# Kernel tuning notes

Hardware: AMD Instinct MI355X
Metric: run time of the kernel (lower is better)

Reference implementation:

```python
import jax, jax.numpy as jnp
import numpy as np

N_NODES = 100000
N_EDGES = 3200000
NUM_GRAPHS = 2048
IN_CH = 35
HID = 128
EPS = 1e-5


def setup_inputs() -> dict:
    key = jax.random.key(0)
    ks = jax.random.split(key, 16)
    x = jax.random.normal(ks[0], (N_NODES, IN_CH), dtype=jnp.float32)
    edge_index = jax.random.randint(ks[1], (2, N_EDGES), 0, N_NODES, dtype=jnp.int64)
    batch = jnp.sort(jax.random.randint(ks[2], (N_NODES,), 0, NUM_GRAPHS, dtype=jnp.int64))
    def lin(k, fan_in, fan_out):
        b = 1.0 / np.sqrt(fan_in)
        kw, kb = jax.random.split(k)
        W = jax.random.uniform(kw, (fan_in, fan_out), minval=-b, maxval=b, dtype=jnp.float32)
        bias = jax.random.uniform(kb, (fan_out,), minval=-b, maxval=b, dtype=jnp.float32)
        return W, bias
    W1, b1 = lin(ks[3], IN_CH, HID)
    W2, b2 = lin(ks[4], HID, HID)
    W3, b3 = lin(ks[5], HID, HID)
    Wl1, bl1 = lin(ks[6], HID, HID // 2)
    Wl2, bl2 = lin(ks[7], HID // 2, 1)
    ones = jnp.ones((HID,), jnp.float32)
    zeros = jnp.zeros((HID,), jnp.float32)
    return {
        'x': x, 'edge_index': edge_index, 'batch': batch,
        'W1': W1, 'b1': b1, 'g1': ones, 'be1': zeros,
        'W2': W2, 'b2': b2, 'g2': ones, 'be2': zeros,
        'W3': W3, 'b3': b3, 'g3': ones, 'be3': zeros,
        'Wl1': Wl1, 'bl1': bl1, 'Wl2': Wl2, 'bl2': bl2,
    }


def _gcn_norm(edge_index, n):
    # add self-loops, compute symmetric normalization D^-1/2 (A+I) D^-1/2
    loop = jnp.arange(n, dtype=edge_index.dtype)
    src = jnp.concatenate([edge_index[0], loop])
    dst = jnp.concatenate([edge_index[1], loop])
    deg = jax.ops.segment_sum(jnp.ones_like(dst, jnp.float32), dst, num_segments=n)
    dinv = jnp.where(deg > 0, jax.lax.rsqrt(deg), 0.0)
    norm = dinv[src] * dinv[dst]
    return src, dst, norm


def _gcn_conv(x, src, dst, norm, W, b):
    h = x @ W                      # [N, out]
    msg = h[src] * norm[:, None]   # gather + scale (irregular)
    out = jax.ops.segment_sum(msg, dst, num_segments=x.shape[0])
    return out + b


def _bn(x, g, be):
    mu = jnp.mean(x, axis=0)
    var = jnp.mean(jnp.square(x - mu), axis=0)  # biased var (torch BN training)
    return (x - mu) * jax.lax.rsqrt(var + EPS) * g + be


def reference(x, edge_index, batch, W1, b1, g1, be1, W2, b2, g2, be2,
              W3, b3, g3, be3, Wl1, bl1, Wl2, bl2):
    n = x.shape[0]
    src, dst, norm = _gcn_norm(edge_index, n)
    h = jax.nn.gelu(_bn(_gcn_conv(x, src, dst, norm, W1, b1), g1, be1), approximate=False)
    h = jax.nn.gelu(_bn(_gcn_conv(h, src, dst, norm, W2, b2), g2, be2), approximate=False)
    h = jax.nn.gelu(_bn(_gcn_conv(h, src, dst, norm, W3, b3), g3, be3), approximate=False)
    # global mean pool by graph id
    s = jax.ops.segment_sum(h, batch, num_segments=NUM_GRAPHS)
    cnt = jax.ops.segment_sum(jnp.ones((n,), jnp.float32), batch, num_segments=NUM_GRAPHS)
    pooled = s / jnp.maximum(cnt, 1.0)[:, None]
    out = jax.nn.elu(pooled @ Wl1 + bl1)
    out = out @ Wl2 + bl2
    return out  # [NUM_GRAPHS, 1]
```

## Files before the change

### kernel.cpp

```cpp
#include <hip/hip_runtime.h>
#include <hip/hip_bf16.h>
#include <math.h>

#define N_NODES 100000
#define N_EDGES 3200000
#define NUM_GRAPHS 2048
#define IN_CH 35
#define HID 128
#define BN_EPS 1e-5f

#define BUCK_SHIFT 9
#define BUCK_SIZE 512
#define NB_BUCK 196
#define BIN_GRID 1024
#define BIN_CHUNK 3125

__device__ __forceinline__ float gelu_f(float x) {
    return 0.5f * x * (1.0f + erff(x * 0.70710678118654752440f));
}

__device__ __forceinline__ float bflo(unsigned v) { return __uint_as_float(v << 16); }
__device__ __forceinline__ float bfhi(unsigned v) { return __uint_as_float(v & 0xffff0000u); }
__device__ __forceinline__ unsigned f2bf(float f) {
    unsigned x = __float_as_uint(f);
    return (x + 0x7fffu + ((x >> 16) & 1u)) >> 16;
}
__device__ __forceinline__ unsigned packbf2(float lo, float hi) {
    return f2bf(lo) | (f2bf(hi) << 16);
}


__global__ void k_zero2(int* __restrict__ bcnt, float* __restrict__ stats,
                        unsigned* __restrict__ xzero, unsigned* __restrict__ hzero) {
    int i = threadIdx.x;
    if (i < NB_BUCK) bcnt[i] = 0;
    if (i < 3 * 256) stats[i] = 0.0f;
    if (i < 32) xzero[i] = 0u;
    if (i < 64) hzero[i] = 0u;
}


__global__ void k_bhist(const int* __restrict__ ei, int* __restrict__ bcnt) {
    __shared__ int hist[NB_BUCK];
    int tid = threadIdx.x;
    if (tid < NB_BUCK) hist[tid] = 0;
    __syncthreads();
    int e0 = blockIdx.x * BIN_CHUNK;
    int e1 = min(e0 + BIN_CHUNK, N_EDGES);
    for (int e = e0 + tid; e < e1; e += 256) {
        int d = ei[N_EDGES + e];
        atomicAdd(&hist[d >> BUCK_SHIFT], 1);
    }
    __syncthreads();
    if (tid < NB_BUCK && hist[tid] > 0) atomicAdd(&bcnt[tid], hist[tid]);
}


__global__ void k_bscan(const int* __restrict__ bcnt, int* __restrict__ bbase,
                        int* __restrict__ bcursor, int* __restrict__ rowp) {
    __shared__ int sa[256];
    __shared__ int sb[256];
    int tid = threadIdx.x;
    sa[tid] = (tid < NB_BUCK) ? bcnt[tid] : 0;
    __syncthreads();
    int* src = sa; int* dst = sb;
    for (int st = 1; st < 256; st <<= 1) {
        int v = src[tid];
        if (tid >= st) v += src[tid - st];
        dst[tid] = v;
        __syncthreads();
        int* t = src; src = dst; dst = t;
    }
    if (tid < NB_BUCK) {
        int ex = (tid == 0) ? 0 : src[tid - 1];
        bbase[tid] = ex;
        bcursor[tid] = ex;
    }
    if (tid == 0) {
        bbase[NB_BUCK] = N_EDGES;
        rowp[N_NODES] = N_EDGES;
    }
}


__global__ void k_bin(const int* __restrict__ ei, int* __restrict__ bcursor,
                      int2* __restrict__ edges) {
    __shared__ int lsrc[BIN_CHUNK];
    __shared__ int ldst[BIN_CHUNK];
    __shared__ int hist[NB_BUCK];
    __shared__ int hbase[NB_BUCK];
    __shared__ int lcur[NB_BUCK];
    int tid = threadIdx.x;
    if (tid < NB_BUCK) { hist[tid] = 0; lcur[tid] = 0; }
    __syncthreads();
    int e0 = blockIdx.x * BIN_CHUNK;
    int nE = min(e0 + BIN_CHUNK, N_EDGES) - e0;
    for (int i = tid; i < nE; i += 256) {
        int s = ei[e0 + i];
        int d = ei[N_EDGES + e0 + i];
        lsrc[i] = s;
        ldst[i] = d;
        atomicAdd(&hist[d >> BUCK_SHIFT], 1);
    }
    __syncthreads();
    if (tid < NB_BUCK) {
        int h = hist[tid];
        hbase[tid] = (h > 0) ? atomicAdd(&bcursor[tid], h) : 0;
    }
    __syncthreads();
    for (int i = tid; i < nE; i += 256) {
        int d = ldst[i];
        int b = d >> BUCK_SHIFT;
        int off = atomicAdd(&lcur[b], 1);
        edges[hbase[b] + off] = make_int2(lsrc[i], d);
    }
}


__global__ void k_fill(const int* __restrict__ bbase, const int2* __restrict__ edges,
                       int* __restrict__ rowp, float* __restrict__ dinv,
                       int* __restrict__ col) {
    __shared__ int ldeg[BUCK_SIZE];
    __shared__ int sa[BUCK_SIZE];
    __shared__ int sb[BUCK_SIZE];
    __shared__ int lcur[BUCK_SIZE];
    int b = blockIdx.x;
    int tid = threadIdx.x;
    int base_node = b << BUCK_SHIFT;
    int nn = min(BUCK_SIZE, N_NODES - base_node);
    int seg0 = bbase[b];
    int seg1 = bbase[b + 1];
    ldeg[tid] = 0;
    __syncthreads();
    for (int e = seg0 + tid; e < seg1; e += BUCK_SIZE) {
        atomicAdd(&ldeg[edges[e].y - base_node], 1);
    }
    __syncthreads();
    sa[tid] = ldeg[tid];
    __syncthreads();
    int* src = sa; int* dst = sb;
    for (int st = 1; st < BUCK_SIZE; st <<= 1) {
        int v = src[tid];
        if (tid >= st) v += src[tid - st];
        dst[tid] = v;
        __syncthreads();
        int* t = src; src = dst; dst = t;
    }
    int ex = (tid == 0) ? 0 : src[tid - 1];
    int rp = seg0 + ex;
    lcur[tid] = rp;
    if (tid < nn) {
        rowp[base_node + tid] = rp;
        dinv[base_node + tid] = rsqrtf((float)(ldeg[tid] + 1));
    }
    __syncthreads();
    for (int e = seg0 + tid; e < seg1; e += BUCK_SIZE) {
        int2 sd = edges[e];
        int p = atomicAdd(&lcur[sd.y - base_node], 1);
        col[p] = sd.x;
    }
}


__global__ void k_castx(const float* __restrict__ X, const float* __restrict__ dinv,
                        unsigned* __restrict__ Xb) {
    int i = blockIdx.x * blockDim.x + threadIdx.x;
    if (i >= N_NODES * 32) return;
    int n = i >> 5, j = i & 31;
    float dv = dinv[n];
    float lo = 0.0f, hi = 0.0f;
    if (j < 17) {
        lo = X[(size_t)n * IN_CH + 2 * j];
        hi = X[(size_t)n * IN_CH + 2 * j + 1];
    } else if (j == 17) {
        lo = X[(size_t)n * IN_CH + 34];
    }
    Xb[i] = packbf2(dv * lo, dv * hi);
}

#define ACC8(v) { a0 += bflo(v.x); a1 += bfhi(v.x); a2 += bflo(v.y); a3 += bfhi(v.y); \
                  a4 += bflo(v.z); a5 += bfhi(v.z); a6 += bflo(v.w); a7 += bfhi(v.w); }
#define ACC4(v) { a0 += bflo(v.x); a1 += bfhi(v.x); a2 += bflo(v.y); a3 += bfhi(v.y); }


#define C1_NODES 8

__global__ __launch_bounds__(512) void k_conv1(
        const unsigned* __restrict__ Xb, const int* __restrict__ rowp,
        const int* __restrict__ col, const float* __restrict__ dinv,
        const float* __restrict__ W1, const float* __restrict__ b1,
        unsigned* __restrict__ Yb) {
    __shared__ float w_s[IN_CH * HID];
    __shared__ float b_s[HID];
    __shared__ float xa_s[C1_NODES][36];
    int tid = threadIdx.x;
    for (int u = tid; u < IN_CH * HID; u += 512) w_s[u] = W1[u];
    if (tid < HID) b_s[tid] = b1[tid];

    int wid = tid >> 6;
    int lane = tid & 63;
    int g = lane >> 4;
    int j = lane & 15;
    int node = blockIdx.x * C1_NODES + wid;
    bool valid = node < N_NODES;

    float a0 = 0.0f, a1 = 0.0f, a2 = 0.0f, a3 = 0.0f;
    float di = 0.0f;
    if (valid) {
        int rp0 = rowp[node], rp1 = rowp[node + 1];
        di = dinv[node];
        uint2 sv = *(const uint2*)(Xb + (size_t)node * 32 + j * 2);
        float w0 = (g == 0) ? 1.0f : 0.0f;
        a0 = w0 * bflo(sv.x); a1 = w0 * bfhi(sv.x);
        a2 = w0 * bflo(sv.y); a3 = w0 * bfhi(sv.y);
        unsigned deg = (unsigned)(rp1 - rp0);
        for (int e0 = (rp0 & ~3); e0 < rp1; e0 += 16) {
            int eb = e0 + 4 * g;
            int4 cs = *(const int4*)(col + eb);
            int s0 = ((unsigned)(eb + 0 - rp0) < deg) ? cs.x : N_NODES;
            int s1 = ((unsigned)(eb + 1 - rp0) < deg) ? cs.y : N_NODES;
            int s2 = ((unsigned)(eb + 2 - rp0) < deg) ? cs.z : N_NODES;
            int s3 = ((unsigned)(eb + 3 - rp0) < deg) ? cs.w : N_NODES;
            uint2 v0 = *(const uint2*)(Xb + (size_t)s0 * 32 + j * 2);
            uint2 v1 = *(const uint2*)(Xb + (size_t)s1 * 32 + j * 2);
            uint2 v2 = *(const uint2*)(Xb + (size_t)s2 * 32 + j * 2);
            uint2 v3 = *(const uint2*)(Xb + (size_t)s3 * 32 + j * 2);
            ACC4(v0); ACC4(v1); ACC4(v2); ACC4(v3);
        }
    }
    a0 += __shfl(a0, (lane + 32) & 63, 64);
    a1 += __shfl(a1, (lane + 32) & 63, 64);
    a2 += __shfl(a2, (lane + 32) & 63, 64);
    a3 += __shfl(a3, (lane + 32) & 63, 64);
    a0 += __shfl(a0, (lane + 16) & 63, 64);
    a1 += __shfl(a1, (lane + 16) & 63, 64);
    a2 += __shfl(a2, (lane + 16) & 63, 64);
    a3 += __shfl(a3, (lane + 16) & 63, 64);
    if (valid && g == 0 && j < 9) {
        xa_s[wid][4 * j + 0] = di * a0;
        xa_s[wid][4 * j + 1] = di * a1;
        xa_s[wid][4 * j + 2] = di * a2;
        xa_s[wid][4 * j + 3] = di * a3;
    }
    __syncthreads();
    float acc0 = b_s[2 * lane];
    float acc1 = b_s[2 * lane + 1];
    #pragma unroll 7
    for (int k = 0; k < IN_CH; ++k) {
        float xv = xa_s[wid][k];
        acc0 = fmaf(xv, w_s[k * HID + 2 * lane], acc0);
        acc1 = fmaf(xv, w_s[k * HID + 2 * lane + 1], acc1);
    }
    if (valid) Yb[(size_t)node * 64 + lane] = packbf2(acc0, acc1);
}


__global__ void k_gemm128(const unsigned* __restrict__ Yb, const float* __restrict__ stats,
                          const float* __restrict__ g, const float* __restrict__ be,
                          const float* __restrict__ W, const float* __restrict__ dinv,
                          unsigned* __restrict__ Hb) {
    __shared__ float xs[32 * HID];
    __shared__ float sc_s[HID];
    __shared__ float sh_s[HID];
    int tid = threadIdx.x;
    if (tid < HID) {
        const float inv_n = 1.0f / (float)N_NODES;
        float mean = stats[tid] * inv_n;
        float var = stats[HID + tid] * inv_n - mean * mean;
        float s = g[tid] * rsqrtf(var + BN_EPS);
        sc_s[tid] = s;
        sh_s[tid] = be[tid] - mean * s;
    }
    __syncthreads();
    int row0 = blockIdx.x * 32;
    for (int u = tid; u < 32 * 64; u += 256) {
        int r = u >> 6, p = u & 63;
        int gr = row0 + r;
        float lo = 0.0f, hi = 0.0f;
        if (gr < N_NODES) {
            unsigned v = Yb[(size_t)gr * 64 + p];
            lo = gelu_f(fmaf(bflo(v), sc_s[2 * p], sh_s[2 * p]));
            hi = gelu_f(fmaf(bfhi(v), sc_s[2 * p + 1], sh_s[2 * p + 1]));
        }
        xs[r * HID + 2 * p]     = lo;
        xs[r * HID + 2 * p + 1] = hi;
    }
    __syncthreads();
    int tx = tid & 31, ty = tid >> 5;
    float acc[4][4] = {};
    for (int k = 0; k < HID; ++k) {
        float4 w = *(const float4*)&W[k * HID + tx * 4];
        #pragma unroll
        for (int rr = 0; rr < 4; ++rr) {
            float x = xs[(ty * 4 + rr) * HID + k];
            acc[rr][0] = fmaf(x, w.x, acc[rr][0]);
            acc[rr][1] = fmaf(x, w.y, acc[rr][1]);
            acc[rr][2] = fmaf(x, w.z, acc[rr][2]);
            acc[rr][3] = fmaf(x, w.w, acc[rr][3]);
        }
    }
    #pragma unroll
    for (int rr = 0; rr < 4; ++rr) {
        int gr = row0 + ty * 4 + rr;
        if (gr < N_NODES) {
            float dv = dinv[gr];
            unsigned lo = packbf2(dv * acc[rr][0], dv * acc[rr][1]);
            unsigned hi = packbf2(dv * acc[rr][2], dv * acc[rr][3]);
            *(uint2*)&Hb[(size_t)gr * 64 + tx * 2] = make_uint2(lo, hi);
        }
    }
}


__global__ void k_convb(const unsigned* __restrict__ Hb, const int* __restrict__ rowp,
                        const int* __restrict__ col, const float* __restrict__ dinv,
                        const float* __restrict__ bias, unsigned* __restrict__ Yb) {
    int tid = threadIdx.x;
    int wid = tid >> 6;
    int lane = tid & 63;
    int g = lane >> 4;
    int j = lane & 15;
    int node = blockIdx.x * 4 + wid;
    if (node >= N_NODES) return;
    int rp0 = rowp[node], rp1 = rowp[node + 1];
    float di = dinv[node];
    uint4 sv = *(const uint4*)(Hb + (size_t)node * 64 + j * 4);
    float w0 = (g == 0) ? 1.0f : 0.0f;
    float a0 = w0 * bflo(sv.x), a1 = w0 * bfhi(sv.x);
    float a2 = w0 * bflo(sv.y), a3 = w0 * bfhi(sv.y);
    float a4 = w0 * bflo(sv.z), a5 = w0 * bfhi(sv.z);
    float a6 = w0 * bflo(sv.w), a7 = w0 * bfhi(sv.w);
    unsigned deg = (unsigned)(rp1 - rp0);
    for (int e0 = (rp0 & ~3); e0 < rp1; e0 += 16) {
        int eb = e0 + 4 * g;
        int4 cs = *(const int4*)(col + eb);
        int s0 = ((unsigned)(eb + 0 - rp0) < deg) ? cs.x : N_NODES;
        int s1 = ((unsigned)(eb + 1 - rp0) < deg) ? cs.y : N_NODES;
        int s2 = ((unsigned)(eb + 2 - rp0) < deg) ? cs.z : N_NODES;
        int s3 = ((unsigned)(eb + 3 - rp0) < deg) ? cs.w : N_NODES;
        uint4 v0 = *(const uint4*)(Hb + (size_t)s0 * 64 + j * 4);
        uint4 v1 = *(const uint4*)(Hb + (size_t)s1 * 64 + j * 4);
        uint4 v2 = *(const uint4*)(Hb + (size_t)s2 * 64 + j * 4);
        uint4 v3 = *(const uint4*)(Hb + (size_t)s3 * 64 + j * 4);
        ACC8(v0); ACC8(v1); ACC8(v2); ACC8(v3);
    }
    a0 += __shfl(a0, (lane + 32) & 63, 64);
    a1 += __shfl(a1, (lane + 32) & 63, 64);
    a2 += __shfl(a2, (lane + 32) & 63, 64);
    a3 += __shfl(a3, (lane + 32) & 63, 64);
    a4 += __shfl(a4, (lane + 32) & 63, 64);
    a5 += __shfl(a5, (lane + 32) & 63, 64);
    a6 += __shfl(a6, (lane + 32) & 63, 64);
    a7 += __shfl(a7, (lane + 32) & 63, 64);
    a0 += __shfl(a0, (lane + 16) & 63, 64);
    a1 += __shfl(a1, (lane + 16) & 63, 64);
    a2 += __shfl(a2, (lane + 16) & 63, 64);
    a3 += __shfl(a3, (lane + 16) & 63, 64);
    a4 += __shfl(a4, (lane + 16) & 63, 64);
    a5 += __shfl(a5, (lane + 16) & 63, 64);
    a6 += __shfl(a6, (lane + 16) & 63, 64);
    a7 += __shfl(a7, (lane + 16) & 63, 64);
    if (g == 0) {
        const float4* bp = (const float4*)(bias + 8 * j);
        float4 bA = bp[0], bB = bp[1];
        uint4 o;
        o.x = packbf2(fmaf(di, a0, bA.x), fmaf(di, a1, bA.y));
        o.y = packbf2(fmaf(di, a2, bA.z), fmaf(di, a3, bA.w));
        o.z = packbf2(fmaf(di, a4, bB.x), fmaf(di, a5, bB.y));
        o.w = packbf2(fmaf(di, a6, bB.z), fmaf(di, a7, bB.w));
        *(uint4*)(Yb + (size_t)node * 64 + j * 4) = o;
    }
}


__global__ void k_statsb(const unsigned* __restrict__ Yb, float* __restrict__ stats) {
    __shared__ float ls[128];
    __shared__ float lss[128];
    int tid = threadIdx.x;
    int lane = tid & 63, grp = tid >> 6;
    if (tid < 128) { ls[tid] = 0.0f; lss[tid] = 0.0f; }
    __syncthreads();
    float s0 = 0, s1 = 0, q0 = 0, q1 = 0;
    for (int r = blockIdx.x * 4 + grp; r < N_NODES; r += gridDim.x * 4) {
        unsigned v = Yb[(size_t)r * 64 + lane];
        float lo = bflo(v), hi = bfhi(v);
        s0 += lo; q0 = fmaf(lo, lo, q0);
        s1 += hi; q1 = fmaf(hi, hi, q1);
    }
    atomicAdd(&ls[2 * lane], s0);
    atomicAdd(&ls[2 * lane + 1], s1);
    atomicAdd(&lss[2 * lane], q0);
    atomicAdd(&lss[2 * lane + 1], q1);
    __syncthreads();
    if (tid < 128) {
        atomicAdd(&stats[tid], ls[tid]);
        atomicAdd(&stats[128 + tid], lss[tid]);
    }
}


__device__ __forceinline__ int lowerb(const int* __restrict__ arr, int n, int key) {
    int lo = 0, hi = n;
    while (lo < hi) {
        int mid = (lo + hi) >> 1;
        if (arr[mid] < key) lo = mid + 1; else hi = mid;
    }
    return lo;
}

__global__ void k_pool_mlp(const unsigned* __restrict__ Yb, const float* __restrict__ stats,
                           const float* __restrict__ g, const float* __restrict__ be,
                           const int* __restrict__ batch,
                           const float* __restrict__ Wl1, const float* __restrict__ bl1,
                           const float* __restrict__ Wl2, const float* __restrict__ bl2,
                           float* __restrict__ out) {
    __shared__ float pooled[128];
    __shared__ float sc_s[128];
    __shared__ float sh_s[128];
    __shared__ int bounds[2];
    int gidx = blockIdx.x;
    int tid = threadIdx.x;
    if (tid < 128) {
        const float inv_n = 1.0f / (float)N_NODES;
        float mean = stats[tid] * inv_n;
        float var = stats[128 + tid] * inv_n - mean * mean;
        float s = g[tid] * rsqrtf(var + BN_EPS);
        sc_s[tid] = s;
        sh_s[tid] = be[tid] - mean * s;
    }
    if (tid == 0) {
        bounds[0] = lowerb(batch, N_NODES, gidx);
        bounds[1] = lowerb(batch, N_NODES, gidx + 1);
    }
    __syncthreads();
    int lo = bounds[0], hi = bounds[1];
    float s = sc_s[tid], h = sh_s[tid];
    int half = tid & 1;
    int word = tid >> 1;
    float acc = 0.0f;
    for (int r = lo; r < hi; ++r) {
        unsigned v = Yb[(size_t)r * 64 + word];
        float x = half ? bfhi(v) : bflo(v);
        acc += gelu_f(fmaf(x, s, h));
    }
    pooled[tid] = (hi > lo) ? acc / (float)(hi - lo) : 0.0f;
    __syncthreads();
    if (tid < 64) {
        float hs = bl1[tid];
        #pragma unroll 4
        for (int k = 0; k < 128; ++k)
            hs = fmaf(pooled[k], Wl1[k * 64 + tid], hs);
        float e = (hs > 0.0f) ? hs : expm1f(hs);
        float part = e * Wl2[tid];
        #pragma unroll
        for (int o = 32; o > 0; o >>= 1)
            part += __shfl_down(part, o);
        if (tid == 0) out[gidx] = part + bl2[0];
    }
}


extern "C" void kernel_launch(void* const* d_in, const int* in_sizes, int n_in,
                              void* d_out, int out_size, void* d_ws, size_t ws_size,
                              hipStream_t stream) {
    const float* x   = (const float*)d_in[0];
    const int*   ei  = (const int*)d_in[1];
    const int*   bat = (const int*)d_in[2];
    const float* W1  = (const float*)d_in[3];
    const float* b1  = (const float*)d_in[4];
    const float* g1  = (const float*)d_in[5];
    const float* be1 = (const float*)d_in[6];
    const float* W2  = (const float*)d_in[7];
    const float* b2  = (const float*)d_in[8];
    const float* g2  = (const float*)d_in[9];
    const float* be2 = (const float*)d_in[10];
    const float* W3  = (const float*)d_in[11];
    const float* b3  = (const float*)d_in[12];
    const float* g3  = (const float*)d_in[13];
    const float* be3 = (const float*)d_in[14];
    const float* Wl1 = (const float*)d_in[15];
    const float* bl1 = (const float*)d_in[16];
    const float* Wl2 = (const float*)d_in[17];
    const float* bl2 = (const float*)d_in[18];
    float* out = (float*)d_out;

    char* ws = (char*)d_ws;
    size_t off = 0;
    auto alloc = [&](size_t bytes) -> char* {
        char* p = ws + off;
        off += (bytes + 255) & ~(size_t)255;
        return p;
    };
    int*      bcnt    = (int*)alloc(NB_BUCK * sizeof(int));
    int*      bbase   = (int*)alloc((NB_BUCK + 1) * sizeof(int));
    int*      bcursor = (int*)alloc(NB_BUCK * sizeof(int));
    int2*     edges   = (int2*)alloc((size_t)N_EDGES * sizeof(int2));
    int*      rowp    = (int*)alloc((N_NODES + 1) * sizeof(int));
    float*    dinv    = (float*)alloc(N_NODES * sizeof(float));
    int*      col     = (int*)alloc((size_t)N_EDGES * sizeof(int));
    unsigned* Xb      = (unsigned*)alloc((size_t)(N_NODES + 1) * 32 * sizeof(unsigned));
    unsigned* Ybuf    = (unsigned*)alloc((size_t)N_NODES * 64 * sizeof(unsigned));
    unsigned* Hbuf    = (unsigned*)alloc((size_t)(N_NODES + 1) * 64 * sizeof(unsigned));
    float*    stats   = (float*)alloc(3 * 256 * sizeof(float));

    k_zero2<<<1, 1024, 0, stream>>>(bcnt, stats, Xb + (size_t)N_NODES * 32,
                                    Hbuf + (size_t)N_NODES * 64);
    k_bhist<<<BIN_GRID, 256, 0, stream>>>(ei, bcnt);
    k_bscan<<<1, 256, 0, stream>>>(bcnt, bbase, bcursor, rowp);
    k_bin<<<BIN_GRID, 256, 0, stream>>>(ei, bcursor, edges);
    k_fill<<<NB_BUCK, BUCK_SIZE, 0, stream>>>(bbase, edges, rowp, dinv, col);
    k_castx<<<(N_NODES * 32 + 255) / 256, 256, 0, stream>>>(x, dinv, Xb);

    const int gemm_blocks = (N_NODES + 31) / 32;
    const int conv_blocks = (N_NODES + 3) / 4;

    k_conv1<<<(N_NODES + C1_NODES - 1) / C1_NODES, 512, 0, stream>>>(
        Xb, rowp, col, dinv, W1, b1, Ybuf);
    k_statsb<<<1024, 256, 0, stream>>>(Ybuf, stats + 0 * 256);

    k_gemm128<<<gemm_blocks, 256, 0, stream>>>(Ybuf, stats + 0 * 256, g1, be1, W2, dinv, Hbuf);
    k_convb<<<conv_blocks, 256, 0, stream>>>(Hbuf, rowp, col, dinv, b2, Ybuf);
    k_statsb<<<1024, 256, 0, stream>>>(Ybuf, stats + 1 * 256);

    k_gemm128<<<gemm_blocks, 256, 0, stream>>>(Ybuf, stats + 1 * 256, g2, be2, W3, dinv, Hbuf);
    k_convb<<<conv_blocks, 256, 0, stream>>>(Hbuf, rowp, col, dinv, b3, Ybuf);
    k_statsb<<<1024, 256, 0, stream>>>(Ybuf, stats + 2 * 256);

    k_pool_mlp<<<NUM_GRAPHS, 128, 0, stream>>>(Ybuf, stats + 2 * 256, g3, be3, bat,
                                               Wl1, bl1, Wl2, bl2, out);
}
```

Measured before the change: 792.9 us.

## Use bf16 MFMA for hidden-layer GEMMs with pre-transposed bf16 weights

Replaces the scalar fp32 FMA 128x128 GEMM with a 64-row tile using the mfma_f32_16x16x32_bf16 instruction. BN+GELU activations are packed to bf16 into swizzled shared memory. Weights are cast and transposed once into bf16 by a new small kernel. This cuts the compute cost of the two GEMM stages. In exchange the weights lose precision to bf16 and the output stores are 16-bit scattered writes.

```diff
diff --git a/kernel.cpp b/kernel.cpp
--- a/kernel.cpp
+++ b/kernel.cpp
@@ -14,6 +14,9 @@
 #define NB_BUCK 196
 #define BIN_GRID 1024
 #define BIN_CHUNK 3125
+
+typedef short bf16x8 __attribute__((ext_vector_type(8)));
+typedef float f32x4 __attribute__((ext_vector_type(4)));
 
 __device__ __forceinline__ float gelu_f(float x) {
     return 0.5f * x * (1.0f + erff(x * 0.70710678118654752440f));
@@ -37,6 +40,18 @@
     if (i < 3 * 256) stats[i] = 0.0f;
     if (i < 32) xzero[i] = 0u;
     if (i < 64) hzero[i] = 0u;
+}
+
+
+__global__ void k_wcast(const float* __restrict__ W2, const float* __restrict__ W3,
+                        unsigned* __restrict__ Wt2, unsigned* __restrict__ Wt3) {
+    int t = blockIdx.x * 256 + threadIdx.x;
+    if (t >= 2 * 8192) return;
+    const float* W = (t < 8192) ? W2 : W3;
+    unsigned* Wt = (t < 8192) ? Wt2 : Wt3;
+    int i = t & 8191;
+    int n = i >> 6, j = i & 63;
+    Wt[n * 64 + j] = packbf2(W[(2 * j) * HID + n], W[(2 * j + 1) * HID + n]);
 }
 
 
@@ -255,11 +270,12 @@
 }
 
 
-__global__ void k_gemm128(const unsigned* __restrict__ Yb, const float* __restrict__ stats,
-                          const float* __restrict__ g, const float* __restrict__ be,
-                          const float* __restrict__ W, const float* __restrict__ dinv,
-                          unsigned* __restrict__ Hb) {
-    __shared__ float xs[32 * HID];
+__global__ __launch_bounds__(256) void k_gemm128m(
+        const unsigned* __restrict__ Yb, const float* __restrict__ stats,
+        const float* __restrict__ g, const float* __restrict__ be,
+        const unsigned* __restrict__ Wt, const float* __restrict__ dinv,
+        unsigned* __restrict__ Hb) {
+    __shared__ __align__(16) unsigned act[64 * 64];
     __shared__ float sc_s[HID];
     __shared__ float sh_s[HID];
     int tid = threadIdx.x;
@@ -272,41 +288,57 @@
         sh_s[tid] = be[tid] - mean * s;
     }
     __syncthreads();
-    int row0 = blockIdx.x * 32;
-    for (int u = tid; u < 32 * 64; u += 256) {
-        int r = u >> 6, p = u & 63;
+    int row0 = blockIdx.x * 64;
+    #pragma unroll
+    for (int it = 0; it < 8; ++it) {
+        int idx = it * 256 + tid;
+        int r = idx >> 5;
+        int c2 = idx & 31;
         int gr = row0 + r;
-        float lo = 0.0f, hi = 0.0f;
-        if (gr < N_NODES) {
-            unsigned v = Yb[(size_t)gr * 64 + p];
-            lo = gelu_f(fmaf(bflo(v), sc_s[2 * p], sh_s[2 * p]));
-            hi = gelu_f(fmaf(bfhi(v), sc_s[2 * p + 1], sh_s[2 * p + 1]));
+        uint2 v = make_uint2(0u, 0u);
+        if (gr < N_NODES) v = *(const uint2*)(Yb + (size_t)gr * 64 + c2 * 2);
+        int c = c2 * 2;
+        float x0 = gelu_f(fmaf(bflo(v.x), sc_s[2 * c], sh_s[2 * c]));
+        float x1 = gelu_f(fmaf(bfhi(v.x), sc_s[2 * c + 1], sh_s[2 * c + 1]));
+        float x2 = gelu_f(fmaf(bflo(v.y), sc_s[2 * c + 2], sh_s[2 * c + 2]));
+        float x3 = gelu_f(fmaf(bfhi(v.y), sc_s[2 * c + 3], sh_s[2 * c + 3]));
+        int swz = (r & 7) << 2;
+        act[r * 64 + (c ^ swz)]       = packbf2(x0, x1);
+        act[r * 64 + ((c + 1) ^ swz)] = packbf2(x2, x3);
+    }
+    __syncthreads();
+    int l = tid & 63;
+    int w = tid >> 6;
+    int r0 = w * 16;
+    int arow = r0 + (l & 15);
+    int kgrp = l >> 4;
+    bf16x8 afrag[4];
+    #pragma unroll
+    for (int kk = 0; kk < 4; ++kk) {
+        int base = (kk * 16 + kgrp * 4) ^ ((arow & 7) << 2);
+        afrag[kk] = *(const bf16x8*)&act[arow * 64 + base];
+    }
+    float dv[4];
+    #pragma unroll
+    for (int reg = 0; reg < 4; ++reg) {
+        int gr = row0 + r0 + kgrp * 4 + reg;
+        dv[reg] = (gr < N_NODES) ? dinv[gr] : 0.0f;
+    }
+    unsigned short* Hb16 = (unsigned short*)Hb;
+    #pragma unroll
+    for (int n0 = 0; n0 < 8; ++n0) {
+        f32x4 acc = {0.0f, 0.0f, 0.0f, 0.0f};
+        #pragma unroll
+        for (int kk = 0; kk < 4; ++kk) {
+            bf16x8 b = *(const bf16x8*)&Wt[(n0 * 16 + (l & 15)) * 64 + kk * 16 + kgrp * 4];
+            acc = __builtin_amdgcn_mfma_f32_16x16x32_bf16(afrag[kk], b, acc, 0, 0, 0);
         }
-        xs[r * HID + 2 * p]     = lo;
-        xs[r * HID + 2 * p + 1] = hi;
-    }
-    __syncthreads();
-    int tx = tid & 31, ty = tid >> 5;
-    float acc[4][4] = {};
-    for (int k = 0; k < HID; ++k) {
-        float4 w = *(const float4*)&W[k * HID + tx * 4];
+        int colg = n0 * 16 + (l & 15);
         #pragma unroll
-        for (int rr = 0; rr < 4; ++rr) {
-            float x = xs[(ty * 4 + rr) * HID + k];
-            acc[rr][0] = fmaf(x, w.x, acc[rr][0]);
-            acc[rr][1] = fmaf(x, w.y, acc[rr][1]);
-            acc[rr][2] = fmaf(x, w.z, acc[rr][2]);
-            acc[rr][3] = fmaf(x, w.w, acc[rr][3]);
-        }
-    }
-    #pragma unroll
-    for (int rr = 0; rr < 4; ++rr) {
-        int gr = row0 + ty * 4 + rr;
-        if (gr < N_NODES) {
-            float dv = dinv[gr];
-            unsigned lo = packbf2(dv * acc[rr][0], dv * acc[rr][1]);
-            unsigned hi = packbf2(dv * acc[rr][2], dv * acc[rr][3]);
-            *(uint2*)&Hb[(size_t)gr * 64 + tx * 2] = make_uint2(lo, hi);
+        for (int reg = 0; reg < 4; ++reg) {
+            int gr = row0 + r0 + kgrp * 4 + reg;
+            if (gr < N_NODES)
+                Hb16[(size_t)gr * HID + colg] = (unsigned short)f2bf(dv[reg] * acc[reg]);
         }
     }
 }
@@ -502,27 +534,30 @@
     unsigned* Ybuf    = (unsigned*)alloc((size_t)N_NODES * 64 * sizeof(unsigned));
     unsigned* Hbuf    = (unsigned*)alloc((size_t)(N_NODES + 1) * 64 * sizeof(unsigned));
     float*    stats   = (float*)alloc(3 * 256 * sizeof(float));
+    unsigned* Wt2     = (unsigned*)alloc(8192 * sizeof(unsigned));
+    unsigned* Wt3     = (unsigned*)alloc(8192 * sizeof(unsigned));
 
     k_zero2<<<1, 1024, 0, stream>>>(bcnt, stats, Xb + (size_t)N_NODES * 32,
                                     Hbuf + (size_t)N_NODES * 64);
+    k_wcast<<<64, 256, 0, stream>>>(W2, W3, Wt2, Wt3);
     k_bhist<<<BIN_GRID, 256, 0, stream>>>(ei, bcnt);
     k_bscan<<<1, 256, 0, stream>>>(bcnt, bbase, bcursor, rowp);
     k_bin<<<BIN_GRID, 256, 0, stream>>>(ei, bcursor, edges);
     k_fill<<<NB_BUCK, BUCK_SIZE, 0, stream>>>(bbase, edges, rowp, dinv, col);
     k_castx<<<(N_NODES * 32 + 255) / 256, 256, 0, stream>>>(x, dinv, Xb);
 
-    const int gemm_blocks = (N_NODES + 31) / 32;
+    const int gemm_blocks = (N_NODES + 63) / 64;
     const int conv_blocks = (N_NODES + 3) / 4;
 
     k_conv1<<<(N_NODES + C1_NODES - 1) / C1_NODES, 512, 0, stream>>>(
         Xb, rowp, col, dinv, W1, b1, Ybuf);
     k_statsb<<<1024, 256, 0, stream>>>(Ybuf, stats + 0 * 256);
 
-    k_gemm128<<<gemm_blocks, 256, 0, stream>>>(Ybuf, stats + 0 * 256, g1, be1, W2, dinv, Hbuf);
+    k_gemm128m<<<gemm_blocks, 256, 0, stream>>>(Ybuf, stats + 0 * 256, g1, be1, Wt2, dinv, Hbuf);
     k_convb<<<conv_blocks, 256, 0, stream>>>(Hbuf, rowp, col, dinv, b2, Ybuf);
     k_statsb<<<1024, 256, 0, stream>>>(Ybuf, stats + 1 * 256);
 
-    k_gemm128<<<gemm_blocks, 256, 0, stream>>>(Ybuf, stats + 1 * 256, g2, be2, W3, dinv, Hbuf);
+    k_gemm128m<<<gemm_blocks, 256, 0, stream>>>(Ybuf, stats + 1 * 256, g2, be2, Wt3, dinv, Hbuf);
     k_convb<<<conv_blocks, 256, 0, stream>>>(Hbuf, rowp, col, dinv, b3, Ybuf);
     k_statsb<<<1024, 256, 0, stream>>>(Ybuf, stats + 2 * 256);
 
```

After: 740.5 us. -6.6%, faster.
